# Optimization experiments

Hardware: AMD Instinct MI355X
Metric: run time of the kernel (lower is better)

The kernel has to match this reference:

```python
import jax, jax.numpy as jnp
import numpy as np

B, T, E, H, TAG = 32, 1024, 512, 512, 2


def setup_inputs() -> dict:
    key = jax.random.key(0)
    ks = jax.random.split(key, 10)
    s = 1.0 / np.sqrt(H)
    u = lambda k, shape: jax.random.uniform(k, shape, jnp.float32, -s, s)
    xs = jax.random.normal(ks[0], (B, T, E), jnp.float32)
    lengths = jnp.sort(jax.random.randint(ks[1], (B,), 1, T + 1))[::-1]  # pack_padded wants descending
    domains = jnp.ones((B,), jnp.int32)  # single-domain path -> plain model + classification
    return dict(
        xs=xs, lengths=lengths, domains=domains,
        w_ih_f=u(ks[2], (4 * H, E)), w_hh_f=u(ks[3], (4 * H, H)), b_f=u(ks[4], (4 * H,)),
        w_ih_b=u(ks[5], (4 * H, E)), w_hh_b=u(ks[6], (4 * H, H)), b_b=u(ks[7], (4 * H,)),
        w_cls=u(ks[8], (TAG, 2 * H)), b_cls=u(ks[9], (TAG,)),
    )


def _run_lstm(xw, mask, w_hh):
    # xw: [T,B,4H] precomputed x @ W_ih^T + b ; mask: [T,B,1] valid positions
    Hd = w_hh.shape[1]
    Bn = xw.shape[1]

    def step(carry, inp):
        h, c = carry
        xw_t, m = inp
        g = xw_t + h @ w_hh.T                         # [B,4H], torch gate order i,f,g,o
        i, f, gg, o = jnp.split(g, 4, axis=-1)
        c_new = jax.nn.sigmoid(f) * c + jax.nn.sigmoid(i) * jnp.tanh(gg)
        h_new = jax.nn.sigmoid(o) * jnp.tanh(c_new)
        h = jnp.where(m, h_new, h)                    # packed seq: state frozen past length
        c = jnp.where(m, c_new, c)
        return (h, c), h_new * m                      # padded output is zero past length

    init = (jnp.zeros((Bn, Hd), xw.dtype), jnp.zeros((Bn, Hd), xw.dtype))
    _, outs = jax.lax.scan(step, init, (xw, mask))
    return outs  # [T,B,H]


def reference(xs, lengths, domains, w_ih_f, w_hh_f, b_f, w_ih_b, w_hh_b, b_b, w_cls, b_cls):
    Bn, Tn, _ = xs.shape
    t = jnp.arange(Tn)
    mask = (t[:, None] < lengths[None, :])[:, :, None]            # [T,B,1]
    # forward direction
    xw_f = jnp.einsum('bte,ge->tbg', xs, w_ih_f) + b_f
    out_f = _run_lstm(xw_f, mask, w_hh_f)                          # [T,B,H]
    # backward direction: reverse the valid prefix of each sequence
    idx = jnp.where(t[None, :] < lengths[:, None],
                    lengths[:, None] - 1 - t[None, :], t[None, :])  # [B,T]
    xs_rev = jnp.take_along_axis(xs, idx[:, :, None], axis=1)
    xw_b = jnp.einsum('bte,ge->tbg', xs_rev, w_ih_b) + b_b
    out_b_rev = _run_lstm(xw_b, mask, w_hh_b)                      # [T,B,H]
    out_b = jnp.take_along_axis(out_b_rev.transpose(1, 0, 2), idx[:, :, None], axis=1)
    out_b = out_b * mask.transpose(1, 0, 2)                        # zero padded positions
    h = jnp.concatenate([out_f.transpose(1, 0, 2), out_b], axis=-1)  # [B,T,2H]
    logits = h @ w_cls.T + b_cls                                   # [B,T,TAG]
    return jax.nn.softmax(logits, axis=2)
```

## Files before the change

kernel.cpp:

```cpp
#include <hip/hip_runtime.h>
#include <math.h>

#define B_N 32
#define T_N 1024
#define E_N 512
#define H_N 512
#define G4_N 2048

typedef __attribute__((ext_vector_type(8))) short short8;
typedef __attribute__((ext_vector_type(4))) float f32x4;
typedef __attribute__((ext_vector_type(4))) unsigned int uint32x4;
typedef unsigned long long ull;

__device__ __forceinline__ unsigned short f2bfu(float f) {
  unsigned int x = __builtin_bit_cast(unsigned int, f);
  x += 0x7fffu + ((x >> 16) & 1u);
  return (unsigned short)(x >> 16);
}
__device__ __forceinline__ float bfu2f(unsigned short u) {
  return __builtin_bit_cast(float, ((unsigned int)u) << 16);
}
__device__ __forceinline__ float sigmf(float x) { return 1.0f / (1.0f + expf(-x)); }

__device__ __forceinline__ void load64_mall(const unsigned short* p,
                                            uint32x4& a, uint32x4& b,
                                            uint32x4& c, uint32x4& d) {
  asm volatile("global_load_dwordx4 %0, %4, off sc0 sc1\n\t"
               "global_load_dwordx4 %1, %4, off offset:16 sc0 sc1\n\t"
               "global_load_dwordx4 %2, %4, off offset:32 sc0 sc1\n\t"
               "global_load_dwordx4 %3, %4, off offset:48 sc0 sc1\n\t"
               "s_waitcnt vmcnt(0)"
               : "=&v"(a), "=&v"(b), "=&v"(c), "=&v"(d)
               : "v"(p) : "memory");
}
__device__ __forceinline__ void store32_mall(unsigned int* p, unsigned int v) {
  asm volatile("global_store_dword %0, %1, off sc0 sc1" :: "v"(p), "v"(v) : "memory");
}

__device__ __forceinline__ void poll_flag2(const unsigned int* pf, unsigned int want) {
  unsigned int fa, fb;
  asm volatile("global_load_dword %0, %2, off sc0 sc1\n\t"
               "global_load_dword %1, %2, off sc0 sc1"
               : "=&v"(fa), "=&v"(fb) : "v"(pf) : "memory");
  for (;;) {
    asm volatile("s_waitcnt vmcnt(1)" ::: "memory");
    __builtin_amdgcn_sched_barrier(0);
    if (fa >= want) break;
    asm volatile("global_load_dword %0, %1, off sc0 sc1" : "=&v"(fa) : "v"(pf) : "memory");
    asm volatile("s_waitcnt vmcnt(1)" ::: "memory");
    __builtin_amdgcn_sched_barrier(0);
    if (fb >= want) break;
    asm volatile("global_load_dword %0, %1, off sc0 sc1" : "=&v"(fb) : "v"(pf) : "memory");
  }
}

__global__ __launch_bounds__(256) void xw_gemm_kernel(
    const float* __restrict__ xs, const int* __restrict__ lengths,
    const float* __restrict__ w_ih_f, const float* __restrict__ b_f,
    const float* __restrict__ w_ih_b, const float* __restrict__ b_b,
    unsigned short* __restrict__ xw, int t0, int Tseg)
{
  __shared__ unsigned short As[64][80];
  __shared__ unsigned short Bs[64][80];
  const int g0 = blockIdx.x * 64;
  const int n0 = blockIdx.y * 64;
  const int dir = blockIdx.z;
  const float* __restrict__ W = dir ? w_ih_b : w_ih_f;
  const float* __restrict__ bias = dir ? b_b : b_f;
  const int tid = threadIdx.x;
  const int w = tid >> 6, lane = tid & 63;
  const int wr = w >> 1, wc = w & 1;

  const int sr = tid >> 2;
  const int sq = tid & 3;
  const int nrow = n0 + sr;
  const int bb = nrow & 31;
  const int tt = t0 + (nrow >> 5);
  const int Lb = lengths[bb];
  const int src_t = (dir != 0 && tt < Lb) ? (Lb - 1 - tt) : tt;
  const float* __restrict__ xrow = xs + ((size_t)bb * T_N + src_t) * E_N;
  const float* __restrict__ arow = W + (size_t)(g0 + sr) * E_N;

  f32x4 acc[2][2] = {};

  for (int k0 = 0; k0 < E_N; k0 += 64) {
    float4 av[4], bv[4];
#pragma unroll
    for (int i = 0; i < 4; ++i) {
      av[i] = *(const float4*)&arow[k0 + sq * 16 + i * 4];
      bv[i] = *(const float4*)&xrow[k0 + sq * 16 + i * 4];
    }
    __syncthreads();
#pragma unroll
    for (int i = 0; i < 4; ++i) {
      ushort4 a4, b4;
      a4.x = f2bfu(av[i].x); a4.y = f2bfu(av[i].y); a4.z = f2bfu(av[i].z); a4.w = f2bfu(av[i].w);
      b4.x = f2bfu(bv[i].x); b4.y = f2bfu(bv[i].y); b4.z = f2bfu(bv[i].z); b4.w = f2bfu(bv[i].w);
      *(ushort4*)&As[sr][sq * 16 + i * 4] = a4;
      *(ushort4*)&Bs[sr][sq * 16 + i * 4] = b4;
    }
    __syncthreads();
#pragma unroll
    for (int kk = 0; kk < 2; ++kk) {
      const int ko = kk * 32 + ((lane >> 4) << 3);
      short8 bf0 = *(const short8*)&Bs[wc * 32 + (lane & 15)][ko];
      short8 bf1 = *(const short8*)&Bs[wc * 32 + 16 + (lane & 15)][ko];
      short8 af0 = *(const short8*)&As[wr * 32 + (lane & 15)][ko];
      short8 af1 = *(const short8*)&As[wr * 32 + 16 + (lane & 15)][ko];
      acc[0][0] = __builtin_amdgcn_mfma_f32_16x16x32_bf16(af0, bf0, acc[0][0], 0, 0, 0);
      acc[0][1] = __builtin_amdgcn_mfma_f32_16x16x32_bf16(af0, bf1, acc[0][1], 0, 0, 0);
      acc[1][0] = __builtin_amdgcn_mfma_f32_16x16x32_bf16(af1, bf0, acc[1][0], 0, 0, 0);
      acc[1][1] = __builtin_amdgcn_mfma_f32_16x16x32_bf16(af1, bf1, acc[1][1], 0, 0, 0);
    }
  }

#pragma unroll
  for (int mt = 0; mt < 2; ++mt)
#pragma unroll
    for (int nt = 0; nt < 2; ++nt)
#pragma unroll
      for (int j = 0; j < 4; ++j) {
        const int m = g0 + wr * 32 + mt * 16 + ((lane >> 4) << 2) + j;
        const int n = n0 + wc * 32 + nt * 16 + (lane & 15);
        const int tl = n >> 5, b = n & 31;
        const float v = acc[mt][nt][j] + bias[m];
        xw[(((size_t)dir * Tseg + tl) * G4_N + m) * B_N + b] = f2bfu(v);
      }
}

__global__ __launch_bounds__(512, 1) void rec_kernel(
    const unsigned short* __restrict__ xw,
    const float* __restrict__ w_hh_f, const float* __restrict__ w_hh_b,
    const float* __restrict__ w_cls, const int* __restrict__ lengths,
    unsigned short* __restrict__ hx,
    unsigned int* __restrict__ flg,
    float* __restrict__ c_buf,
    float* __restrict__ lpart,
    int t0, int Tseg)
{
  __shared__ unsigned short Ah[32][520];
  __shared__ float gate_p[8][32][17];
  __shared__ float lp[16][33][2];

  const int tid = threadIdx.x;
  const int wg = blockIdx.x;
  const int dir = wg & 1;
  const int cg = wg >> 1;
  const int colbase = cg * 16;
  const float* __restrict__ w_hh = dir ? w_hh_b : w_hh_f;
  const int w = tid >> 6, lane = tid & 63;
  const int q = w >> 1, kh = w & 1;

  short8 wfrag[8];
  {
    const int grow = q * 512 + colbase + (lane & 15);
    const int kb = (lane >> 4) << 3;
    const float* __restrict__ wr_ = &w_hh[(size_t)grow * H_N + kh * 256];
#pragma unroll
    for (int ks = 0; ks < 8; ++ks) {
      const float4 f0 = *(const float4*)&wr_[ks * 32 + kb];
      const float4 f1 = *(const float4*)&wr_[ks * 32 + kb + 4];
      short8 v;
      v[0] = (short)f2bfu(f0.x); v[1] = (short)f2bfu(f0.y);
      v[2] = (short)f2bfu(f0.z); v[3] = (short)f2bfu(f0.w);
      v[4] = (short)f2bfu(f1.x); v[5] = (short)f2bfu(f1.y);
      v[6] = (short)f2bfu(f1.z); v[7] = (short)f2bfu(f1.w);
      wfrag[ks] = v;
    }
  }

  const int b = tid >> 4;
  const int cl = tid & 15;
  const int col = colbase + cl;
  const int Lb = lengths[b];
  const int Lb_r = lengths[tid & 31];
  float cc = c_buf[((size_t)dir * B_N + b) * H_N + col];
  const float wc0 = w_cls[dir * H_N + col];
  const float wc1 = w_cls[2 * H_N + dir * H_N + col];

  float hh = bfu2f(hx[((size_t)dir * 2 + (t0 & 1)) * 16384 + ((size_t)cg * 32 + b) * 16 + cl]);

  float* __restrict__ lslice = lpart + (size_t)wg * B_N * T_N * 2;
  unsigned int* __restrict__ myflag = flg + ((size_t)dir * 32 + cg) * 8 + w;
  const unsigned int* __restrict__ pollflag =
      flg + ((size_t)dir * 32 + (tid >> 4)) * 8 + ((tid & 15) >> 1);

  unsigned short xv[4];
  {
    const unsigned short* __restrict__ xb =
        &xw[((size_t)(dir * Tseg) * G4_N + colbase + cl) * B_N + b];
#pragma unroll
    for (int q2 = 0; q2 < 4; ++q2) xv[q2] = xb[(size_t)q2 * 512 * B_N];
  }

  const int b0 = (tid & 15) * 2, cg16 = (tid >> 4) * 16;

  for (int ts = 0; ts < Tseg; ++ts) {
    const int t = t0 + ts;

    poll_flag2(pollflag, (unsigned int)t);
    {
      uint32x4 va, vb, vc, vd;
      load64_mall(hx + ((size_t)dir * 2 + (t & 1)) * 16384 + (size_t)tid * 32,
                  va, vb, vc, vd);
      *(uint32x4*)&Ah[b0][cg16] = va;
      *(uint32x4*)&Ah[b0][cg16 + 8] = vb;
      *(uint32x4*)&Ah[b0 + 1][cg16] = vc;
      *(uint32x4*)&Ah[b0 + 1][cg16 + 8] = vd;
    }
    __syncthreads();

    if (ts > 0 && tid < 64) {
      const int br = tid & 31, tau = tid >> 5;
      const int tp = t - 1;
      if (tp < Lb_r) {
        float s = 0.f;
#pragma unroll
        for (int k = 0; k < 16; ++k) s += lp[k][br][tau];
        const int tpos = dir ? (Lb_r - 1 - tp) : tp;
        lslice[((size_t)br * T_N + tpos) * 2 + tau] = s;
      }
    }

    {
      f32x4 acc0 = {0.f, 0.f, 0.f, 0.f}, acc1 = {0.f, 0.f, 0.f, 0.f};
      const int kb = (lane >> 4) << 3;
#pragma unroll
      for (int ks = 0; ks < 8; ++ks) {
        const int kk = kh * 256 + (ks << 5) + kb;
        short8 a0 = *(const short8*)&Ah[(lane & 15)][kk];
        short8 a1 = *(const short8*)&Ah[16 + (lane & 15)][kk];
        acc0 = __builtin_amdgcn_mfma_f32_16x16x32_bf16(a0, wfrag[ks], acc0, 0, 0, 0);
        acc1 = __builtin_amdgcn_mfma_f32_16x16x32_bf16(a1, wfrag[ks], acc1, 0, 0, 0);
      }
      const int crow = (lane >> 4) << 2;
      const int ccol = lane & 15;
#pragma unroll
      for (int j = 0; j < 4; ++j) {
        gate_p[w][crow + j][ccol] = acc0[j];
        gate_p[w][16 + crow + j][ccol] = acc1[j];
      }
    }
    __syncthreads();

    const bool valid = (t < Lb);
    float hn;
    {
      const float gi = gate_p[0][b][cl] + gate_p[1][b][cl] + bfu2f(xv[0]);
      const float gf = gate_p[2][b][cl] + gate_p[3][b][cl] + bfu2f(xv[1]);
      const float gg = gate_p[4][b][cl] + gate_p[5][b][cl] + bfu2f(xv[2]);
      const float go = gate_p[6][b][cl] + gate_p[7][b][cl] + bfu2f(xv[3]);
      const float cn = sigmf(gf) * cc + sigmf(gi) * tanhf(gg);
      hn = sigmf(go) * tanhf(cn);
      if (valid) { cc = cn; hh = hn; }
    }

    {
      const float hhp = __shfl_xor(hh, 1);
      if ((cl & 1) == 0) {
        const unsigned int pv =
            (unsigned int)f2bfu(hh) | ((unsigned int)f2bfu(hhp) << 16);
        store32_mall((unsigned int*)(hx + ((size_t)dir * 2 + ((t + 1) & 1)) * 16384 +
                                     ((size_t)cg * 32 + b) * 16 + cl),
                     pv);
      }
    }
    lp[cl][b][0] = valid ? hn * wc0 : 0.f;
    lp[cl][b][1] = valid ? hn * wc1 : 0.f;

    asm volatile("s_waitcnt vmcnt(0)" ::: "memory");
    __builtin_amdgcn_sched_barrier(0);
    if (lane == 0)
      store32_mall(myflag, (unsigned int)(t + 1));

    if (ts + 1 < Tseg) {
      const unsigned short* __restrict__ xb =
          &xw[((size_t)(dir * Tseg + ts + 1) * G4_N + colbase + cl) * B_N + b];
#pragma unroll
      for (int q2 = 0; q2 < 4; ++q2) xv[q2] = xb[(size_t)q2 * 512 * B_N];
    }
  }

  if (tid < 64) {
    const int br = tid & 31, tau = tid >> 5;
    const int tp = t0 + Tseg - 1;
    if (tp < Lb_r) {
      float s = 0.f;
#pragma unroll
      for (int k = 0; k < 16; ++k) s += lp[k][br][tau];
      const int tpos = dir ? (Lb_r - 1 - tp) : tp;
      lslice[((size_t)br * T_N + tpos) * 2 + tau] = s;
    }
  }

  c_buf[((size_t)dir * B_N + b) * H_N + col] = cc;
}

__global__ void init_kernel(ull* __restrict__ hx64, float* __restrict__ c_buf,
                            unsigned int* __restrict__ flg)
{
  const int i = blockIdx.x * 256 + threadIdx.x;
  if (i < 16384) hx64[i] = 0ull;
  if (i < 2 * B_N * H_N) c_buf[i] = 0.f;
  if (i < 1024) flg[i] = 0u;
}

__global__ void reduce_softmax_kernel(const float* __restrict__ lpart,
                                      const float* __restrict__ b_cls,
                                      float* __restrict__ out)
{
  const int i = blockIdx.x * 256 + threadIdx.x;
  if (i >= B_N * T_N) return;
  float s0 = b_cls[0], s1 = b_cls[1];
  const float* __restrict__ p = lpart + (size_t)i * 2;
#pragma unroll 8
  for (int wg = 0; wg < 64; ++wg) {
    s0 += p[(size_t)wg * B_N * T_N * 2];
    s1 += p[(size_t)wg * B_N * T_N * 2 + 1];
  }
  const float m = fmaxf(s0, s1);
  const float e0 = expf(s0 - m), e1 = expf(s1 - m);
  const float inv = 1.f / (e0 + e1);
  out[2 * i] = e0 * inv;
  out[2 * i + 1] = e1 * inv;
}

extern "C" void kernel_launch(void* const* d_in, const int* in_sizes, int n_in,
                              void* d_out, int out_size, void* d_ws, size_t ws_size,
                              hipStream_t stream)
{
  const float* xs      = (const float*)d_in[0];
  const int*   lengths = (const int*)d_in[1];
  const float* w_ih_f  = (const float*)d_in[3];
  const float* w_hh_f  = (const float*)d_in[4];
  const float* b_f     = (const float*)d_in[5];
  const float* w_ih_b  = (const float*)d_in[6];
  const float* w_hh_b  = (const float*)d_in[7];
  const float* b_b     = (const float*)d_in[8];
  const float* w_cls   = (const float*)d_in[9];
  const float* b_cls   = (const float*)d_in[10];
  float* out = (float*)d_out;

  auto alignup = [](size_t v) { return (v + 255) & ~(size_t)255; };
  const size_t hx_b    = alignup((size_t)2 * 2 * 32 * 32 * 16 * 2);
  const size_t flg_b   = alignup((size_t)1024 * 4);
  const size_t cbuf_b  = alignup((size_t)2 * B_N * H_N * 4);
  const size_t lpart_b = alignup((size_t)64 * B_N * T_N * 2 * 4);
  const size_t fixed = hx_b + flg_b + cbuf_b + lpart_b + 1024;

  int nseg = 1;
  while (nseg < 64) {
    const size_t xwb = alignup((size_t)2 * (T_N / nseg) * G4_N * B_N * 2);
    if (xwb + fixed <= ws_size) break;
    nseg <<= 1;
  }
  const int Tseg = T_N / nseg;
  const size_t xw_b = alignup((size_t)2 * Tseg * G4_N * B_N * 2);

  char* p = (char*)d_ws;
  unsigned short* xw = (unsigned short*)p;  p += xw_b;
  unsigned short* hx = (unsigned short*)p;  p += hx_b;
  unsigned int* flg = (unsigned int*)p;     p += flg_b;
  float* c_buf = (float*)p;                 p += cbuf_b;
  float* lpart = (float*)p;                 p += lpart_b;

  hipMemsetAsync(lpart, 0, lpart_b, stream);
  init_kernel<<<256, 256, 0, stream>>>((ull*)hx, c_buf, flg);

  for (int s = 0; s < nseg; ++s) {
    const int t0 = s * Tseg;
    dim3 g(G4_N / 64, (Tseg * B_N) / 64, 2);
    xw_gemm_kernel<<<g, 256, 0, stream>>>(xs, lengths, w_ih_f, b_f, w_ih_b, b_b, xw, t0, Tseg);
    rec_kernel<<<64, 512, 0, stream>>>(xw, w_hh_f, w_hh_b, w_cls, lengths,
                                       hx, flg, c_buf, lpart, t0, Tseg);
  }

  reduce_softmax_kernel<<<128, 256, 0, stream>>>(lpart, b_cls, out);
}
```

Measured before the change: 4.453 ms.

## Fuse input-projection GEMM into recurrent kernel with counter-based producer/consumer overlap

Merges the xW GEMM and the recurrent LSTM kernel into one launch. 64 blocks run the recurrence while 192 blocks produce the input projections in time order and signal per-timestep-pair counters that the recurrent blocks spin on. The projection layout is changed to interleave the four gates so each recurrent thread fetches them with a single 8-byte load issued alongside the h load. Timesteps past the maximum sequence length are skipped in both the GEMM and the recurrence. This hides GEMM time behind the serial recurrence, at the cost of the recurrent and GEMM blocks needing to be co-resident and of polling traffic.

```diff
diff --git a/kernel.cpp b/kernel.cpp
--- a/kernel.cpp
+++ b/kernel.cpp
@@ -6,6 +6,8 @@
 #define E_N 512
 #define H_N 512
 #define G4_N 2048
+#define NREC 64
+#define NGEMM 192
 
 typedef __attribute__((ext_vector_type(8))) short short8;
 typedef __attribute__((ext_vector_type(4))) float f32x4;
@@ -22,19 +24,24 @@
 }
 __device__ __forceinline__ float sigmf(float x) { return 1.0f / (1.0f + expf(-x)); }
 
-__device__ __forceinline__ void load64_mall(const unsigned short* p,
-                                            uint32x4& a, uint32x4& b,
-                                            uint32x4& c, uint32x4& d) {
-  asm volatile("global_load_dwordx4 %0, %4, off sc0 sc1\n\t"
-               "global_load_dwordx4 %1, %4, off offset:16 sc0 sc1\n\t"
-               "global_load_dwordx4 %2, %4, off offset:32 sc0 sc1\n\t"
-               "global_load_dwordx4 %3, %4, off offset:48 sc0 sc1\n\t"
+__device__ __forceinline__ void load_h_xw(const unsigned short* ph, const unsigned short* px,
+                                          uint32x4& a, uint32x4& b,
+                                          uint32x4& c, uint32x4& d, ull& x) {
+  asm volatile("global_load_dwordx4 %0, %5, off sc0 sc1\n\t"
+               "global_load_dwordx4 %1, %5, off offset:16 sc0 sc1\n\t"
+               "global_load_dwordx4 %2, %5, off offset:32 sc0 sc1\n\t"
+               "global_load_dwordx4 %3, %5, off offset:48 sc0 sc1\n\t"
+               "global_load_dwordx2 %4, %6, off sc0 sc1\n\t"
                "s_waitcnt vmcnt(0)"
-               : "=&v"(a), "=&v"(b), "=&v"(c), "=&v"(d)
-               : "v"(p) : "memory");
+               : "=&v"(a), "=&v"(b), "=&v"(c), "=&v"(d), "=&v"(x)
+               : "v"(ph), "v"(px) : "memory");
 }
 __device__ __forceinline__ void store32_mall(unsigned int* p, unsigned int v) {
   asm volatile("global_store_dword %0, %1, off sc0 sc1" :: "v"(p), "v"(v) : "memory");
+}
+__device__ __forceinline__ void store16_mall(unsigned short* p, unsigned short v) {
+  unsigned int vv = v;
+  asm volatile("global_store_short %0, %1, off sc0 sc1" :: "v"(p), "v"(vv) : "memory");
 }
 
 __device__ __forceinline__ void poll_flag2(const unsigned int* pf, unsigned int want) {
@@ -54,101 +61,107 @@
   }
 }
 
-__global__ __launch_bounds__(256) void xw_gemm_kernel(
+__global__ __launch_bounds__(512, 1) void fused_kernel(
     const float* __restrict__ xs, const int* __restrict__ lengths,
     const float* __restrict__ w_ih_f, const float* __restrict__ b_f,
     const float* __restrict__ w_ih_b, const float* __restrict__ b_b,
-    unsigned short* __restrict__ xw, int t0, int Tseg)
-{
-  __shared__ unsigned short As[64][80];
-  __shared__ unsigned short Bs[64][80];
-  const int g0 = blockIdx.x * 64;
-  const int n0 = blockIdx.y * 64;
-  const int dir = blockIdx.z;
-  const float* __restrict__ W = dir ? w_ih_b : w_ih_f;
-  const float* __restrict__ bias = dir ? b_b : b_f;
-  const int tid = threadIdx.x;
-  const int w = tid >> 6, lane = tid & 63;
-  const int wr = w >> 1, wc = w & 1;
-
-  const int sr = tid >> 2;
-  const int sq = tid & 3;
-  const int nrow = n0 + sr;
-  const int bb = nrow & 31;
-  const int tt = t0 + (nrow >> 5);
-  const int Lb = lengths[bb];
-  const int src_t = (dir != 0 && tt < Lb) ? (Lb - 1 - tt) : tt;
-  const float* __restrict__ xrow = xs + ((size_t)bb * T_N + src_t) * E_N;
-  const float* __restrict__ arow = W + (size_t)(g0 + sr) * E_N;
-
-  f32x4 acc[2][2] = {};
-
-  for (int k0 = 0; k0 < E_N; k0 += 64) {
-    float4 av[4], bv[4];
-#pragma unroll
-    for (int i = 0; i < 4; ++i) {
-      av[i] = *(const float4*)&arow[k0 + sq * 16 + i * 4];
-      bv[i] = *(const float4*)&xrow[k0 + sq * 16 + i * 4];
-    }
-    __syncthreads();
-#pragma unroll
-    for (int i = 0; i < 4; ++i) {
-      ushort4 a4, b4;
-      a4.x = f2bfu(av[i].x); a4.y = f2bfu(av[i].y); a4.z = f2bfu(av[i].z); a4.w = f2bfu(av[i].w);
-      b4.x = f2bfu(bv[i].x); b4.y = f2bfu(bv[i].y); b4.z = f2bfu(bv[i].z); b4.w = f2bfu(bv[i].w);
-      *(ushort4*)&As[sr][sq * 16 + i * 4] = a4;
-      *(ushort4*)&Bs[sr][sq * 16 + i * 4] = b4;
-    }
-    __syncthreads();
-#pragma unroll
-    for (int kk = 0; kk < 2; ++kk) {
-      const int ko = kk * 32 + ((lane >> 4) << 3);
-      short8 bf0 = *(const short8*)&Bs[wc * 32 + (lane & 15)][ko];
-      short8 bf1 = *(const short8*)&Bs[wc * 32 + 16 + (lane & 15)][ko];
-      short8 af0 = *(const short8*)&As[wr * 32 + (lane & 15)][ko];
-      short8 af1 = *(const short8*)&As[wr * 32 + 16 + (lane & 15)][ko];
-      acc[0][0] = __builtin_amdgcn_mfma_f32_16x16x32_bf16(af0, bf0, acc[0][0], 0, 0, 0);
-      acc[0][1] = __builtin_amdgcn_mfma_f32_16x16x32_bf16(af0, bf1, acc[0][1], 0, 0, 0);
-      acc[1][0] = __builtin_amdgcn_mfma_f32_16x16x32_bf16(af1, bf0, acc[1][0], 0, 0, 0);
-      acc[1][1] = __builtin_amdgcn_mfma_f32_16x16x32_bf16(af1, bf1, acc[1][1], 0, 0, 0);
-    }
-  }
-
-#pragma unroll
-  for (int mt = 0; mt < 2; ++mt)
-#pragma unroll
-    for (int nt = 0; nt < 2; ++nt)
-#pragma unroll
-      for (int j = 0; j < 4; ++j) {
-        const int m = g0 + wr * 32 + mt * 16 + ((lane >> 4) << 2) + j;
-        const int n = n0 + wc * 32 + nt * 16 + (lane & 15);
-        const int tl = n >> 5, b = n & 31;
-        const float v = acc[mt][nt][j] + bias[m];
-        xw[(((size_t)dir * Tseg + tl) * G4_N + m) * B_N + b] = f2bfu(v);
-      }
-}
-
-__global__ __launch_bounds__(512, 1) void rec_kernel(
-    const unsigned short* __restrict__ xw,
     const float* __restrict__ w_hh_f, const float* __restrict__ w_hh_b,
-    const float* __restrict__ w_cls, const int* __restrict__ lengths,
+    const float* __restrict__ w_cls,
+    unsigned short* __restrict__ xwp,
     unsigned short* __restrict__ hx,
     unsigned int* __restrict__ flg,
+    unsigned int* __restrict__ cnt,
     float* __restrict__ c_buf,
     float* __restrict__ lpart,
     int t0, int Tseg)
 {
-  __shared__ unsigned short Ah[32][520];
-  __shared__ float gate_p[8][32][17];
-  __shared__ float lp[16][33][2];
-
+  __shared__ alignas(16) unsigned char smem[55296];
   const int tid = threadIdx.x;
+  const int Lmax = lengths[0];
+  const int w = tid >> 6, lane = tid & 63;
+
+  if (blockIdx.x >= NREC) {
+    unsigned short* As = (unsigned short*)smem;
+    unsigned short* Bs = (unsigned short*)(smem + 10240);
+    const int g = blockIdx.x - NREC;
+    const int wr = w >> 2, wc = w & 3;
+    const int sr = tid >> 3, sq = tid & 7;
+    const int ntau = (Tseg >> 1) << 6;
+
+    for (int tau = g; tau < ntau; tau += NGEMM) {
+      const int gtile = tau & 31;
+      const int dir = (tau >> 5) & 1;
+      const int tchunk = tau >> 6;
+      const int tt0g = t0 + tchunk * 2;
+      if (tt0g < Lmax) {
+        const int g0 = gtile * 64;
+        const float* __restrict__ W = dir ? w_ih_b : w_ih_f;
+        const float* __restrict__ bias = dir ? b_b : b_f;
+        const int bb = sr & 31;
+        const int tt = tt0g + (sr >> 5);
+        const int Lb = lengths[bb];
+        const int src_t = (dir != 0 && tt < Lb) ? (Lb - 1 - tt) : tt;
+        const float* __restrict__ xrow = xs + ((size_t)bb * T_N + src_t) * E_N;
+        const float* __restrict__ arow = W + (size_t)(g0 + sr) * E_N;
+        f32x4 accm[2] = {};
+
+        for (int k0 = 0; k0 < E_N; k0 += 64) {
+          const float4 av0 = *(const float4*)&arow[k0 + sq * 8];
+          const float4 av1 = *(const float4*)&arow[k0 + sq * 8 + 4];
+          const float4 bv0 = *(const float4*)&xrow[k0 + sq * 8];
+          const float4 bv1 = *(const float4*)&xrow[k0 + sq * 8 + 4];
+          __syncthreads();
+          ushort4 u;
+          u.x = f2bfu(av0.x); u.y = f2bfu(av0.y); u.z = f2bfu(av0.z); u.w = f2bfu(av0.w);
+          *(ushort4*)&As[sr * 80 + sq * 8] = u;
+          u.x = f2bfu(av1.x); u.y = f2bfu(av1.y); u.z = f2bfu(av1.z); u.w = f2bfu(av1.w);
+          *(ushort4*)&As[sr * 80 + sq * 8 + 4] = u;
+          u.x = f2bfu(bv0.x); u.y = f2bfu(bv0.y); u.z = f2bfu(bv0.z); u.w = f2bfu(bv0.w);
+          *(ushort4*)&Bs[sr * 80 + sq * 8] = u;
+          u.x = f2bfu(bv1.x); u.y = f2bfu(bv1.y); u.z = f2bfu(bv1.z); u.w = f2bfu(bv1.w);
+          *(ushort4*)&Bs[sr * 80 + sq * 8 + 4] = u;
+          __syncthreads();
+#pragma unroll
+          for (int kk = 0; kk < 2; ++kk) {
+            const int ko = kk * 32 + ((lane >> 4) << 3);
+            short8 bf  = *(const short8*)&Bs[(wc * 16 + (lane & 15)) * 80 + ko];
+            short8 af0 = *(const short8*)&As[(wr * 32 + (lane & 15)) * 80 + ko];
+            short8 af1 = *(const short8*)&As[(wr * 32 + 16 + (lane & 15)) * 80 + ko];
+            accm[0] = __builtin_amdgcn_mfma_f32_16x16x32_bf16(af0, bf, accm[0], 0, 0, 0);
+            accm[1] = __builtin_amdgcn_mfma_f32_16x16x32_bf16(af1, bf, accm[1], 0, 0, 0);
+          }
+        }
+#pragma unroll
+        for (int mt = 0; mt < 2; ++mt)
+#pragma unroll
+          for (int j = 0; j < 4; ++j) {
+            const int m = g0 + wr * 32 + mt * 16 + ((lane >> 4) << 2) + j;
+            const int n = tchunk * 64 + wc * 16 + (lane & 15);
+            const int tl = n >> 5, b = n & 31;
+            const int qg = m >> 9, colg = m & 511;
+            const float v = accm[mt][j] + bias[m];
+            store16_mall(&xwp[((((size_t)dir * Tseg + tl) * 512 + colg) * 32 + b) * 4 + qg],
+                         f2bfu(v));
+          }
+        asm volatile("s_waitcnt vmcnt(0)" ::: "memory");
+      }
+      __syncthreads();
+      if (tid == 0 && tt0g < Lmax)
+        __hip_atomic_fetch_add(&cnt[dir * 512 + ((unsigned)tt0g >> 1)], 1u,
+                               __ATOMIC_RELAXED, __HIP_MEMORY_SCOPE_AGENT);
+    }
+    return;
+  }
+
+  unsigned short (*Ah)[520] = (unsigned short (*)[520])smem;
+  float (*gate_p)[32][17] = (float (*)[32][17])(smem + 33280);
+  float (*lp)[33][2] = (float (*)[33][2])(smem + 50688);
+
   const int wg = blockIdx.x;
   const int dir = wg & 1;
   const int cg = wg >> 1;
   const int colbase = cg * 16;
   const float* __restrict__ w_hh = dir ? w_hh_b : w_hh_f;
-  const int w = tid >> 6, lane = tid & 63;
   const int q = w >> 1, kh = w & 1;
 
   short8 wfrag[8];
@@ -177,7 +190,6 @@
   float cc = c_buf[((size_t)dir * B_N + b) * H_N + col];
   const float wc0 = w_cls[dir * H_N + col];
   const float wc1 = w_cls[2 * H_N + dir * H_N + col];
-
   float hh = bfu2f(hx[((size_t)dir * 2 + (t0 & 1)) * 16384 + ((size_t)cg * 32 + b) * 16 + cl]);
 
   float* __restrict__ lslice = lpart + (size_t)wg * B_N * T_N * 2;
@@ -185,24 +197,25 @@
   const unsigned int* __restrict__ pollflag =
       flg + ((size_t)dir * 32 + (tid >> 4)) * 8 + ((tid & 15) >> 1);
 
-  unsigned short xv[4];
-  {
-    const unsigned short* __restrict__ xb =
-        &xw[((size_t)(dir * Tseg) * G4_N + colbase + cl) * B_N + b];
-#pragma unroll
-    for (int q2 = 0; q2 < 4; ++q2) xv[q2] = xb[(size_t)q2 * 512 * B_N];
-  }
-
   const int b0 = (tid & 15) * 2, cg16 = (tid >> 4) * 16;
-
-  for (int ts = 0; ts < Tseg; ++ts) {
+  const int Tloc = min(Tseg, max(0, Lmax - t0));
+
+  for (int ts = 0; ts < Tloc; ++ts) {
     const int t = t0 + ts;
 
+    if ((t & 1) == 0 || ts == 0) {
+      const unsigned int* cp = cnt + dir * 512 + ((unsigned)t >> 1);
+      while (__hip_atomic_load(cp, __ATOMIC_RELAXED, __HIP_MEMORY_SCOPE_AGENT) < 32u) {}
+    }
+
     poll_flag2(pollflag, (unsigned int)t);
+
+    ull xvp;
     {
       uint32x4 va, vb, vc, vd;
-      load64_mall(hx + ((size_t)dir * 2 + (t & 1)) * 16384 + (size_t)tid * 32,
-                  va, vb, vc, vd);
+      load_h_xw(hx + ((size_t)dir * 2 + (t & 1)) * 16384 + (size_t)tid * 32,
+                xwp + ((((size_t)dir * Tseg + ts) * 512 + col) * 32 + b) * 4,
+                va, vb, vc, vd, xvp);
       *(uint32x4*)&Ah[b0][cg16] = va;
       *(uint32x4*)&Ah[b0][cg16 + 8] = vb;
       *(uint32x4*)&Ah[b0 + 1][cg16] = vc;
@@ -246,10 +259,10 @@
     const bool valid = (t < Lb);
     float hn;
     {
-      const float gi = gate_p[0][b][cl] + gate_p[1][b][cl] + bfu2f(xv[0]);
-      const float gf = gate_p[2][b][cl] + gate_p[3][b][cl] + bfu2f(xv[1]);
-      const float gg = gate_p[4][b][cl] + gate_p[5][b][cl] + bfu2f(xv[2]);
-      const float go = gate_p[6][b][cl] + gate_p[7][b][cl] + bfu2f(xv[3]);
+      const float gi = gate_p[0][b][cl] + gate_p[1][b][cl] + bfu2f((unsigned short)(xvp & 0xffffu));
+      const float gf = gate_p[2][b][cl] + gate_p[3][b][cl] + bfu2f((unsigned short)((xvp >> 16) & 0xffffu));
+      const float gg = gate_p[4][b][cl] + gate_p[5][b][cl] + bfu2f((unsigned short)((xvp >> 32) & 0xffffu));
+      const float go = gate_p[6][b][cl] + gate_p[7][b][cl] + bfu2f((unsigned short)((xvp >> 48) & 0xffffu));
       const float cn = sigmf(gf) * cc + sigmf(gi) * tanhf(gg);
       hn = sigmf(go) * tanhf(cn);
       if (valid) { cc = cn; hh = hn; }
@@ -272,18 +285,11 @@
     __builtin_amdgcn_sched_barrier(0);
     if (lane == 0)
       store32_mall(myflag, (unsigned int)(t + 1));
-
-    if (ts + 1 < Tseg) {
-      const unsigned short* __restrict__ xb =
-          &xw[((size_t)(dir * Tseg + ts + 1) * G4_N + colbase + cl) * B_N + b];
-#pragma unroll
-      for (int q2 = 0; q2 < 4; ++q2) xv[q2] = xb[(size_t)q2 * 512 * B_N];
-    }
-  }
-
-  if (tid < 64) {
+  }
+
+  if (Tloc > 0 && tid < 64) {
     const int br = tid & 31, tau = tid >> 5;
-    const int tp = t0 + Tseg - 1;
+    const int tp = t0 + Tloc - 1;
     if (tp < Lb_r) {
       float s = 0.f;
 #pragma unroll
@@ -297,12 +303,14 @@
 }
 
 __global__ void init_kernel(ull* __restrict__ hx64, float* __restrict__ c_buf,
-                            unsigned int* __restrict__ flg)
+                            unsigned int* __restrict__ flg,
+                            unsigned int* __restrict__ cnt)
 {
   const int i = blockIdx.x * 256 + threadIdx.x;
   if (i < 16384) hx64[i] = 0ull;
   if (i < 2 * B_N * H_N) c_buf[i] = 0.f;
   if (i < 1024) flg[i] = 0u;
+  if (i < 1024) cnt[i] = 0u;
 }
 
 __global__ void reduce_softmax_kernel(const float* __restrict__ lpart,
@@ -344,9 +352,10 @@
   auto alignup = [](size_t v) { return (v + 255) & ~(size_t)255; };
   const size_t hx_b    = alignup((size_t)2 * 2 * 32 * 32 * 16 * 2);
   const size_t flg_b   = alignup((size_t)1024 * 4);
+  const size_t cnt_b   = alignup((size_t)1024 * 4);
   const size_t cbuf_b  = alignup((size_t)2 * B_N * H_N * 4);
   const size_t lpart_b = alignup((size_t)64 * B_N * T_N * 2 * 4);
-  const size_t fixed = hx_b + flg_b + cbuf_b + lpart_b + 1024;
+  const size_t fixed = hx_b + flg_b + cnt_b + cbuf_b + lpart_b + 1024;
 
   int nseg = 1;
   while (nseg < 64) {
@@ -358,21 +367,21 @@
   const size_t xw_b = alignup((size_t)2 * Tseg * G4_N * B_N * 2);
 
   char* p = (char*)d_ws;
-  unsigned short* xw = (unsigned short*)p;  p += xw_b;
+  unsigned short* xwp = (unsigned short*)p; p += xw_b;
   unsigned short* hx = (unsigned short*)p;  p += hx_b;
   unsigned int* flg = (unsigned int*)p;     p += flg_b;
+  unsigned int* cnt = (unsigned int*)p;     p += cnt_b;
   float* c_buf = (float*)p;                 p += cbuf_b;
   float* lpart = (float*)p;                 p += lpart_b;
 
   hipMemsetAsync(lpart, 0, lpart_b, stream);
-  init_kernel<<<256, 256, 0, stream>>>((ull*)hx, c_buf, flg);
+  init_kernel<<<256, 256, 0, stream>>>((ull*)hx, c_buf, flg, cnt);
 
   for (int s = 0; s < nseg; ++s) {
     const int t0 = s * Tseg;
-    dim3 g(G4_N / 64, (Tseg * B_N) / 64, 2);
-    xw_gemm_kernel<<<g, 256, 0, stream>>>(xs, lengths, w_ih_f, b_f, w_ih_b, b_b, xw, t0, Tseg);
-    rec_kernel<<<64, 512, 0, stream>>>(xw, w_hh_f, w_hh_b, w_cls, lengths,
-                                       hx, flg, c_buf, lpart, t0, Tseg);
+    fused_kernel<<<NREC + NGEMM, 512, 0, stream>>>(
+        xs, lengths, w_ih_f, b_f, w_ih_b, b_b, w_hh_f, w_hh_b, w_cls,
+        xwp, hx, flg, cnt, c_buf, lpart, t0, Tseg);
   }
 
   reduce_softmax_kernel<<<128, 256, 0, stream>>>(lpart, b_cls, out);
```

Result: slower. 4.691 ms (+5.3%).

## Fuse input projection into persistent recurrent kernel and drop segmented xw buffer

Applied to the files above, without the earlier changes.

Removes the separate x@W_ih GEMM kernel and its bf16 xw workspace, and keeps W_ih fragments in registers inside the recurrent kernel. Each timestep prefetches the next x row into a double-buffered LDS tile and does the input MFMAs next to the hidden-state MFMAs. The step loop runs only up to the longest sequence length. The classifier partial sum is now reduced with wave shuffles instead of an LDS buffer. This avoids the GEMM launch and the xw traffic, but doubles the MFMA work on the serial critical path of each step and raises register and LDS use.

```diff
diff --git a/kernel.cpp b/kernel.cpp
--- a/kernel.cpp
+++ b/kernel.cpp
@@ -5,7 +5,6 @@
 #define T_N 1024
 #define E_N 512
 #define H_N 512
-#define G4_N 2048
 
 typedef __attribute__((ext_vector_type(8))) short short8;
 typedef __attribute__((ext_vector_type(4))) float f32x4;
@@ -36,7 +35,6 @@
 __device__ __forceinline__ void store32_mall(unsigned int* p, unsigned int v) {
   asm volatile("global_store_dword %0, %1, off sc0 sc1" :: "v"(p), "v"(v) : "memory");
 }
-
 __device__ __forceinline__ void poll_flag2(const unsigned int* pf, unsigned int want) {
   unsigned int fa, fb;
   asm volatile("global_load_dword %0, %2, off sc0 sc1\n\t"
@@ -54,93 +52,19 @@
   }
 }
 
-__global__ __launch_bounds__(256) void xw_gemm_kernel(
+__global__ __launch_bounds__(512, 1) void rec_kernel(
     const float* __restrict__ xs, const int* __restrict__ lengths,
     const float* __restrict__ w_ih_f, const float* __restrict__ b_f,
     const float* __restrict__ w_ih_b, const float* __restrict__ b_b,
-    unsigned short* __restrict__ xw, int t0, int Tseg)
-{
-  __shared__ unsigned short As[64][80];
-  __shared__ unsigned short Bs[64][80];
-  const int g0 = blockIdx.x * 64;
-  const int n0 = blockIdx.y * 64;
-  const int dir = blockIdx.z;
-  const float* __restrict__ W = dir ? w_ih_b : w_ih_f;
-  const float* __restrict__ bias = dir ? b_b : b_f;
-  const int tid = threadIdx.x;
-  const int w = tid >> 6, lane = tid & 63;
-  const int wr = w >> 1, wc = w & 1;
-
-  const int sr = tid >> 2;
-  const int sq = tid & 3;
-  const int nrow = n0 + sr;
-  const int bb = nrow & 31;
-  const int tt = t0 + (nrow >> 5);
-  const int Lb = lengths[bb];
-  const int src_t = (dir != 0 && tt < Lb) ? (Lb - 1 - tt) : tt;
-  const float* __restrict__ xrow = xs + ((size_t)bb * T_N + src_t) * E_N;
-  const float* __restrict__ arow = W + (size_t)(g0 + sr) * E_N;
-
-  f32x4 acc[2][2] = {};
-
-  for (int k0 = 0; k0 < E_N; k0 += 64) {
-    float4 av[4], bv[4];
-#pragma unroll
-    for (int i = 0; i < 4; ++i) {
-      av[i] = *(const float4*)&arow[k0 + sq * 16 + i * 4];
-      bv[i] = *(const float4*)&xrow[k0 + sq * 16 + i * 4];
-    }
-    __syncthreads();
-#pragma unroll
-    for (int i = 0; i < 4; ++i) {
-      ushort4 a4, b4;
-      a4.x = f2bfu(av[i].x); a4.y = f2bfu(av[i].y); a4.z = f2bfu(av[i].z); a4.w = f2bfu(av[i].w);
-      b4.x = f2bfu(bv[i].x); b4.y = f2bfu(bv[i].y); b4.z = f2bfu(bv[i].z); b4.w = f2bfu(bv[i].w);
-      *(ushort4*)&As[sr][sq * 16 + i * 4] = a4;
-      *(ushort4*)&Bs[sr][sq * 16 + i * 4] = b4;
-    }
-    __syncthreads();
-#pragma unroll
-    for (int kk = 0; kk < 2; ++kk) {
-      const int ko = kk * 32 + ((lane >> 4) << 3);
-      short8 bf0 = *(const short8*)&Bs[wc * 32 + (lane & 15)][ko];
-      short8 bf1 = *(const short8*)&Bs[wc * 32 + 16 + (lane & 15)][ko];
-      short8 af0 = *(const short8*)&As[wr * 32 + (lane & 15)][ko];
-      short8 af1 = *(const short8*)&As[wr * 32 + 16 + (lane & 15)][ko];
-      acc[0][0] = __builtin_amdgcn_mfma_f32_16x16x32_bf16(af0, bf0, acc[0][0], 0, 0, 0);
-      acc[0][1] = __builtin_amdgcn_mfma_f32_16x16x32_bf16(af0, bf1, acc[0][1], 0, 0, 0);
-      acc[1][0] = __builtin_amdgcn_mfma_f32_16x16x32_bf16(af1, bf0, acc[1][0], 0, 0, 0);
-      acc[1][1] = __builtin_amdgcn_mfma_f32_16x16x32_bf16(af1, bf1, acc[1][1], 0, 0, 0);
-    }
-  }
-
-#pragma unroll
-  for (int mt = 0; mt < 2; ++mt)
-#pragma unroll
-    for (int nt = 0; nt < 2; ++nt)
-#pragma unroll
-      for (int j = 0; j < 4; ++j) {
-        const int m = g0 + wr * 32 + mt * 16 + ((lane >> 4) << 2) + j;
-        const int n = n0 + wc * 32 + nt * 16 + (lane & 15);
-        const int tl = n >> 5, b = n & 31;
-        const float v = acc[mt][nt][j] + bias[m];
-        xw[(((size_t)dir * Tseg + tl) * G4_N + m) * B_N + b] = f2bfu(v);
-      }
-}
-
-__global__ __launch_bounds__(512, 1) void rec_kernel(
-    const unsigned short* __restrict__ xw,
     const float* __restrict__ w_hh_f, const float* __restrict__ w_hh_b,
-    const float* __restrict__ w_cls, const int* __restrict__ lengths,
+    const float* __restrict__ w_cls,
     unsigned short* __restrict__ hx,
     unsigned int* __restrict__ flg,
-    float* __restrict__ c_buf,
-    float* __restrict__ lpart,
-    int t0, int Tseg)
+    float* __restrict__ lpart)
 {
   __shared__ unsigned short Ah[32][520];
+  __shared__ unsigned short Xs2[2][32][520];
   __shared__ float gate_p[8][32][17];
-  __shared__ float lp[16][33][2];
 
   const int tid = threadIdx.x;
   const int wg = blockIdx.x;
@@ -148,24 +72,36 @@
   const int cg = wg >> 1;
   const int colbase = cg * 16;
   const float* __restrict__ w_hh = dir ? w_hh_b : w_hh_f;
+  const float* __restrict__ w_ih = dir ? w_ih_b : w_ih_f;
+  const float* __restrict__ bias = dir ? b_b : b_f;
   const int w = tid >> 6, lane = tid & 63;
   const int q = w >> 1, kh = w & 1;
-
-  short8 wfrag[8];
+  const int Lmax = lengths[0];
+  const int Tloc = (Lmax < T_N) ? Lmax : T_N;
+
+  short8 whh[8], wih[8];
   {
     const int grow = q * 512 + colbase + (lane & 15);
     const int kb = (lane >> 4) << 3;
-    const float* __restrict__ wr_ = &w_hh[(size_t)grow * H_N + kh * 256];
+    const float* __restrict__ rh = &w_hh[(size_t)grow * H_N + kh * 256];
+    const float* __restrict__ ri = &w_ih[(size_t)grow * E_N + kh * 256];
 #pragma unroll
     for (int ks = 0; ks < 8; ++ks) {
-      const float4 f0 = *(const float4*)&wr_[ks * 32 + kb];
-      const float4 f1 = *(const float4*)&wr_[ks * 32 + kb + 4];
+      float4 f0 = *(const float4*)&rh[ks * 32 + kb];
+      float4 f1 = *(const float4*)&rh[ks * 32 + kb + 4];
       short8 v;
       v[0] = (short)f2bfu(f0.x); v[1] = (short)f2bfu(f0.y);
       v[2] = (short)f2bfu(f0.z); v[3] = (short)f2bfu(f0.w);
       v[4] = (short)f2bfu(f1.x); v[5] = (short)f2bfu(f1.y);
       v[6] = (short)f2bfu(f1.z); v[7] = (short)f2bfu(f1.w);
-      wfrag[ks] = v;
+      whh[ks] = v;
+      f0 = *(const float4*)&ri[ks * 32 + kb];
+      f1 = *(const float4*)&ri[ks * 32 + kb + 4];
+      v[0] = (short)f2bfu(f0.x); v[1] = (short)f2bfu(f0.y);
+      v[2] = (short)f2bfu(f0.z); v[3] = (short)f2bfu(f0.w);
+      v[4] = (short)f2bfu(f1.x); v[5] = (short)f2bfu(f1.y);
+      v[6] = (short)f2bfu(f1.z); v[7] = (short)f2bfu(f1.w);
+      wih[ks] = v;
     }
   }
 
@@ -173,30 +109,48 @@
   const int cl = tid & 15;
   const int col = colbase + cl;
   const int Lb = lengths[b];
-  const int Lb_r = lengths[tid & 31];
-  float cc = c_buf[((size_t)dir * B_N + b) * H_N + col];
+  float cc = 0.f, hh = 0.f;
   const float wc0 = w_cls[dir * H_N + col];
   const float wc1 = w_cls[2 * H_N + dir * H_N + col];
-
-  float hh = bfu2f(hx[((size_t)dir * 2 + (t0 & 1)) * 16384 + ((size_t)cg * 32 + b) * 16 + cl]);
+  const float bi  = bias[col];
+  const float bff = bias[512 + col];
+  const float bg  = bias[1024 + col];
+  const float bo  = bias[1536 + col];
 
   float* __restrict__ lslice = lpart + (size_t)wg * B_N * T_N * 2;
   unsigned int* __restrict__ myflag = flg + ((size_t)dir * 32 + cg) * 8 + w;
   const unsigned int* __restrict__ pollflag =
       flg + ((size_t)dir * 32 + (tid >> 4)) * 8 + ((tid & 15) >> 1);
 
-  unsigned short xv[4];
+  const int b0 = (tid & 15) * 2, cg16 = (tid >> 4) * 16;
+
   {
-    const unsigned short* __restrict__ xb =
-        &xw[((size_t)(dir * Tseg) * G4_N + colbase + cl) * B_N + b];
-#pragma unroll
-    for (int q2 = 0; q2 < 4; ++q2) xv[q2] = xb[(size_t)q2 * 512 * B_N];
-  }
-
-  const int b0 = (tid & 15) * 2, cg16 = (tid >> 4) * 16;
-
-  for (int ts = 0; ts < Tseg; ++ts) {
-    const int t = t0 + ts;
+    const int srcT = 0;
+    const int st = dir ? (Lb - 1) : srcT;
+    const float* __restrict__ xrow = xs + ((size_t)b * T_N + st) * E_N + cl * 32;
+    unsigned short* __restrict__ dst = &Xs2[0][b][cl * 32];
+#pragma unroll
+    for (int i = 0; i < 8; ++i) {
+      const float4 v = *(const float4*)&xrow[i * 4];
+      ushort4 u;
+      u.x = f2bfu(v.x); u.y = f2bfu(v.y); u.z = f2bfu(v.z); u.w = f2bfu(v.w);
+      *(ushort4*)&dst[i * 4] = u;
+    }
+  }
+  __syncthreads();
+
+  for (int ts = 0; ts < Tloc; ++ts) {
+    const int t = ts;
+
+    float4 av[8];
+    const bool pfv = (ts + 1 < Tloc);
+    if (pfv) {
+      const int tn = t + 1;
+      const int st = (dir && tn < Lb) ? (Lb - 1 - tn) : tn;
+      const float* __restrict__ xrow = xs + ((size_t)b * T_N + st) * E_N + cl * 32;
+#pragma unroll
+      for (int i = 0; i < 8; ++i) av[i] = *(const float4*)&xrow[i * 4];
+    }
 
     poll_flag2(pollflag, (unsigned int)t);
     {
@@ -210,28 +164,32 @@
     }
     __syncthreads();
 
-    if (ts > 0 && tid < 64) {
-      const int br = tid & 31, tau = tid >> 5;
-      const int tp = t - 1;
-      if (tp < Lb_r) {
-        float s = 0.f;
-#pragma unroll
-        for (int k = 0; k < 16; ++k) s += lp[k][br][tau];
-        const int tpos = dir ? (Lb_r - 1 - tp) : tp;
-        lslice[((size_t)br * T_N + tpos) * 2 + tau] = s;
+    if (pfv) {
+      unsigned short* __restrict__ dst = &Xs2[(t + 1) & 1][b][cl * 32];
+#pragma unroll
+      for (int i = 0; i < 8; ++i) {
+        ushort4 u;
+        u.x = f2bfu(av[i].x); u.y = f2bfu(av[i].y);
+        u.z = f2bfu(av[i].z); u.w = f2bfu(av[i].w);
+        *(ushort4*)&dst[i * 4] = u;
       }
     }
 
     {
       f32x4 acc0 = {0.f, 0.f, 0.f, 0.f}, acc1 = {0.f, 0.f, 0.f, 0.f};
       const int kb = (lane >> 4) << 3;
+      const unsigned short (*Xc)[520] = Xs2[t & 1];
 #pragma unroll
       for (int ks = 0; ks < 8; ++ks) {
         const int kk = kh * 256 + (ks << 5) + kb;
         short8 a0 = *(const short8*)&Ah[(lane & 15)][kk];
         short8 a1 = *(const short8*)&Ah[16 + (lane & 15)][kk];
-        acc0 = __builtin_amdgcn_mfma_f32_16x16x32_bf16(a0, wfrag[ks], acc0, 0, 0, 0);
-        acc1 = __builtin_amdgcn_mfma_f32_16x16x32_bf16(a1, wfrag[ks], acc1, 0, 0, 0);
+        acc0 = __builtin_amdgcn_mfma_f32_16x16x32_bf16(a0, whh[ks], acc0, 0, 0, 0);
+        acc1 = __builtin_amdgcn_mfma_f32_16x16x32_bf16(a1, whh[ks], acc1, 0, 0, 0);
+        short8 x0 = *(const short8*)&Xc[(lane & 15)][kk];
+        short8 x1 = *(const short8*)&Xc[16 + (lane & 15)][kk];
+        acc0 = __builtin_amdgcn_mfma_f32_16x16x32_bf16(x0, wih[ks], acc0, 0, 0, 0);
+        acc1 = __builtin_amdgcn_mfma_f32_16x16x32_bf16(x1, wih[ks], acc1, 0, 0, 0);
       }
       const int crow = (lane >> 4) << 2;
       const int ccol = lane & 15;
@@ -246,10 +204,10 @@
     const bool valid = (t < Lb);
     float hn;
     {
-      const float gi = gate_p[0][b][cl] + gate_p[1][b][cl] + bfu2f(xv[0]);
-      const float gf = gate_p[2][b][cl] + gate_p[3][b][cl] + bfu2f(xv[1]);
-      const float gg = gate_p[4][b][cl] + gate_p[5][b][cl] + bfu2f(xv[2]);
-      const float go = gate_p[6][b][cl] + gate_p[7][b][cl] + bfu2f(xv[3]);
+      const float gi = gate_p[0][b][cl] + gate_p[1][b][cl] + bi;
+      const float gf = gate_p[2][b][cl] + gate_p[3][b][cl] + bff;
+      const float gg = gate_p[4][b][cl] + gate_p[5][b][cl] + bg;
+      const float go = gate_p[6][b][cl] + gate_p[7][b][cl] + bo;
       const float cn = sigmf(gf) * cc + sigmf(gi) * tanhf(gg);
       hn = sigmf(go) * tanhf(cn);
       if (valid) { cc = cn; hh = hn; }
@@ -265,43 +223,32 @@
                      pv);
       }
     }
-    lp[cl][b][0] = valid ? hn * wc0 : 0.f;
-    lp[cl][b][1] = valid ? hn * wc1 : 0.f;
-
     asm volatile("s_waitcnt vmcnt(0)" ::: "memory");
     __builtin_amdgcn_sched_barrier(0);
     if (lane == 0)
       store32_mall(myflag, (unsigned int)(t + 1));
 
-    if (ts + 1 < Tseg) {
-      const unsigned short* __restrict__ xb =
-          &xw[((size_t)(dir * Tseg + ts + 1) * G4_N + colbase + cl) * B_N + b];
-#pragma unroll
-      for (int q2 = 0; q2 < 4; ++q2) xv[q2] = xb[(size_t)q2 * 512 * B_N];
-    }
-  }
-
-  if (tid < 64) {
-    const int br = tid & 31, tau = tid >> 5;
-    const int tp = t0 + Tseg - 1;
-    if (tp < Lb_r) {
-      float s = 0.f;
-#pragma unroll
-      for (int k = 0; k < 16; ++k) s += lp[k][br][tau];
-      const int tpos = dir ? (Lb_r - 1 - tp) : tp;
-      lslice[((size_t)br * T_N + tpos) * 2 + tau] = s;
-    }
-  }
-
-  c_buf[((size_t)dir * B_N + b) * H_N + col] = cc;
-}
-
-__global__ void init_kernel(ull* __restrict__ hx64, float* __restrict__ c_buf,
-                            unsigned int* __restrict__ flg)
+    {
+      float l0 = valid ? hn * wc0 : 0.f;
+      float l1 = valid ? hn * wc1 : 0.f;
+#pragma unroll
+      for (int m = 8; m >= 1; m >>= 1) {
+        l0 += __shfl_xor(l0, m);
+        l1 += __shfl_xor(l1, m);
+      }
+      if (cl == 0 && valid) {
+        const int tpos = dir ? (Lb - 1 - t) : t;
+        float2 v; v.x = l0; v.y = l1;
+        *(float2*)&lslice[((size_t)b * T_N + tpos) * 2] = v;
+      }
+    }
+  }
+}
+
+__global__ void init_kernel(ull* __restrict__ hx64, unsigned int* __restrict__ flg)
 {
   const int i = blockIdx.x * 256 + threadIdx.x;
   if (i < 16384) hx64[i] = 0ull;
-  if (i < 2 * B_N * H_N) c_buf[i] = 0.f;
   if (i < 1024) flg[i] = 0u;
 }
 
@@ -344,36 +291,18 @@
   auto alignup = [](size_t v) { return (v + 255) & ~(size_t)255; };
   const size_t hx_b    = alignup((size_t)2 * 2 * 32 * 32 * 16 * 2);
   const size_t flg_b   = alignup((size_t)1024 * 4);
-  const size_t cbuf_b  = alignup((size_t)2 * B_N * H_N * 4);
   const size_t lpart_b = alignup((size_t)64 * B_N * T_N * 2 * 4);
-  const size_t fixed = hx_b + flg_b + cbuf_b + lpart_b + 1024;
-
-  int nseg = 1;
-  while (nseg < 64) {
-    const size_t xwb = alignup((size_t)2 * (T_N / nseg) * G4_N * B_N * 2);
-    if (xwb + fixed <= ws_size) break;
-    nseg <<= 1;
-  }
-  const int Tseg = T_N / nseg;
-  const size_t xw_b = alignup((size_t)2 * Tseg * G4_N * B_N * 2);
 
   char* p = (char*)d_ws;
-  unsigned short* xw = (unsigned short*)p;  p += xw_b;
   unsigned short* hx = (unsigned short*)p;  p += hx_b;
   unsigned int* flg = (unsigned int*)p;     p += flg_b;
-  float* c_buf = (float*)p;                 p += cbuf_b;
   float* lpart = (float*)p;                 p += lpart_b;
 
   hipMemsetAsync(lpart, 0, lpart_b, stream);
-  init_kernel<<<256, 256, 0, stream>>>((ull*)hx, c_buf, flg);
-
-  for (int s = 0; s < nseg; ++s) {
-    const int t0 = s * Tseg;
-    dim3 g(G4_N / 64, (Tseg * B_N) / 64, 2);
-    xw_gemm_kernel<<<g, 256, 0, stream>>>(xs, lengths, w_ih_f, b_f, w_ih_b, b_b, xw, t0, Tseg);
-    rec_kernel<<<64, 512, 0, stream>>>(xw, w_hh_f, w_hh_b, w_cls, lengths,
-                                       hx, flg, c_buf, lpart, t0, Tseg);
-  }
+  init_kernel<<<64, 256, 0, stream>>>((ull*)hx, flg);
+
+  rec_kernel<<<64, 512, 0, stream>>>(xs, lengths, w_ih_f, b_f, w_ih_b, b_b,
+                                     w_hh_f, w_hh_b, w_cls, hx, flg, lpart);
 
   reduce_softmax_kernel<<<128, 256, 0, stream>>>(lpart, b_cls, out);
 }
```

After: 5.911 ms. 1.33x slower.
